# Kernel optimization log

Measured on AMD Instinct MI355X. Metric: run time of the kernel, lower is better.

Reference implementation:

```python
import jax, jax.numpy as jnp
import numpy as np

D_MODEL, N_HEAD, D_HEAD, D_ROPE = 2048, 16, 128, 64
D_KV, D_Q = 512, 1024
THETA = 10000.0


def _cos_sin(seq_len):
    # freqs_cis equivalent: angles [seq_len, d_rope//2]
    inv = 1.0 / (THETA ** (jnp.arange(0, D_ROPE, 2, dtype=jnp.float32) / D_ROPE))
    ang = jnp.arange(seq_len, dtype=jnp.float32)[:, None] * inv[None, :]
    return jnp.cos(ang), jnp.sin(ang)


def _rope(t, cos, sin):
    # t: [b, s, h, d_rope]; rotate interleaved (even, odd) pairs as complex mult
    t1, t2 = t[..., 0::2], t[..., 1::2]
    c = cos[None, :, None, :]
    s = sin[None, :, None, :]
    out = jnp.stack([t1 * c - t2 * s, t1 * s + t2 * c], axis=-1)
    return out.reshape(t.shape)


def setup_inputs() -> dict:
    key = jax.random.key(0)
    ks = jax.random.split(key, 10)
    b, s = 1, 2048
    x = jax.random.normal(ks[0], (b, s, D_MODEL), dtype=jnp.float32)
    # additive causal mask [s, s]
    mask = jnp.where(jnp.tril(jnp.ones((s, s), dtype=bool)), 0.0, -1e9).astype(jnp.float32)
    def w(k, fan_in, fan_out):
        lim = (6.0 / (fan_in + fan_out)) ** 0.5  # xavier_uniform
        return jax.random.uniform(k, (fan_in, fan_out), jnp.float32, -lim, lim)
    return {
        'x': x, 'mask': mask,
        'W_kv_down': w(ks[1], D_MODEL, D_KV),
        'W_k_up':    w(ks[2], D_KV, N_HEAD * D_HEAD),
        'W_v_up':    w(ks[3], D_KV, N_HEAD * D_HEAD),
        'W_q_down':  w(ks[4], D_MODEL, D_Q),
        'W_q_up':    w(ks[5], D_Q, N_HEAD * D_HEAD),
        'W_q_rope':  w(ks[6], D_Q, N_HEAD * D_ROPE),
        'W_k_rope':  w(ks[7], D_MODEL, N_HEAD * D_ROPE),
        'W_out':     w(ks[8], N_HEAD * D_HEAD, D_MODEL),
    }


def reference(x, mask, W_kv_down, W_k_up, W_v_up, W_q_down, W_q_up, W_q_rope, W_k_rope, W_out):
    b, s, _ = x.shape
    cos, sin = _cos_sin(s)
    # low-rank KV path
    down_kv = x @ W_kv_down                                      # [b,s,d_kv]
    k_c = (down_kv @ W_k_up).reshape(b, s, N_HEAD, D_HEAD)
    v   = (down_kv @ W_v_up).reshape(b, s, N_HEAD, D_HEAD)
    # low-rank Q path
    down_q = x @ W_q_down                                        # [b,s,d_q]
    q_c = (down_q @ W_q_up).reshape(b, s, N_HEAD, D_HEAD)
    q_r = (down_q @ W_q_rope).reshape(b, s, N_HEAD, D_ROPE)
    k_r = (x @ W_k_rope).reshape(b, s, N_HEAD, D_ROPE)
    # decoupled RoPE on rope parts only
    q_r = _rope(q_r, cos, sin)
    k_r = _rope(k_r, cos, sin)
    # concat content + rope, heads to dim 1
    q = jnp.concatenate([q_c, q_r], axis=-1).transpose(0, 2, 1, 3)  # [b,h,s,dh+dr]
    k = jnp.concatenate([k_c, k_r], axis=-1).transpose(0, 2, 1, 3)
    vv = v.transpose(0, 2, 1, 3)                                     # [b,h,s,dh]
    scale = 1.0 / jnp.sqrt(jnp.float32(D_HEAD + D_ROPE))
    scores = jnp.einsum('bhqd,bhkd->bhqk', q, k) * scale + mask[None, None]
    probs = jax.nn.softmax(scores.astype(jnp.float32), axis=-1).astype(q.dtype)
    out = jnp.einsum('bhqk,bhkd->bhqd', probs, vv)                   # [b,h,s,dh]
    out = out.transpose(0, 2, 1, 3).reshape(b, s, N_HEAD * D_HEAD)
    return out @ W_out
```

## Files before the change

kernel.cpp:

```cpp
#include <hip/hip_runtime.h>
#include <hip/hip_bf16.h>
#include <math.h>

#define S 2048
#define DM 2048
#define NH 16
#define DH 128
#define DR 64
#define DKV 512
#define DQ 1024
#define DQK 192
#define QSCALE 0.07216878364870323f

typedef __bf16 bf16x8 __attribute__((ext_vector_type(8)));
typedef float f32x4 __attribute__((ext_vector_type(4)));
typedef unsigned short u16;

__device__ inline unsigned int pack2_bf16(float a, float b) {
    __hip_bfloat16 ha = __float2bfloat16(a);
    __hip_bfloat16 hb = __float2bfloat16(b);
    unsigned short ua = *reinterpret_cast<unsigned short*>(&ha);
    unsigned short ub = *reinterpret_cast<unsigned short*>(&hb);
    return (unsigned int)ua | ((unsigned int)ub << 16);
}
__device__ inline u16 f2bf(float v) {
    __hip_bfloat16 hb = __float2bfloat16(v);
    return *reinterpret_cast<u16*>(&hb);
}
__device__ inline void gload_lds16(const void* g, void* l) {
    __builtin_amdgcn_global_load_lds(
        (const __attribute__((address_space(1))) void*)g,
        (__attribute__((address_space(3))) void*)l, 16, 0, 0);
}

__global__ __launch_bounds__(256) void prep_kernel(
    const float* __restrict__ x,
    const float* __restrict__ W0, const float* __restrict__ W1, const float* __restrict__ W2,
    const float* __restrict__ W3, const float* __restrict__ W4, const float* __restrict__ W5,
    const float* __restrict__ W6, const float* __restrict__ W7,
    u16* __restrict__ x_bf,
    u16* __restrict__ D0, u16* __restrict__ D1, u16* __restrict__ D2, u16* __restrict__ D3,
    u16* __restrict__ D4, u16* __restrict__ D5, u16* __restrict__ D6, u16* __restrict__ D7,
    float* __restrict__ cosT, float* __restrict__ sinT) {
    __shared__ u16 tile[64][65];
    const int b = blockIdx.x;
    if (b < 3584) {
        const float* W; u16* D; int N, K, local;
        if (b < 256)       { W = W0; D = D0; N = 512;  K = 2048; local = b; }
        else if (b < 768)  { W = W1; D = D1; N = 1024; K = 2048; local = b - 256; }
        else if (b < 1280) { W = W2; D = D2; N = 1024; K = 2048; local = b - 768; }
        else if (b < 1536) { W = W3; D = D3; N = 2048; K = 512;  local = b - 1280; }
        else if (b < 1792) { W = W4; D = D4; N = 2048; K = 512;  local = b - 1536; }
        else if (b < 2304) { W = W5; D = D5; N = 2048; K = 1024; local = b - 1792; }
        else if (b < 2560) { W = W6; D = D6; N = 1024; K = 1024; local = b - 2304; }
        else               { W = W7; D = D7; N = 2048; K = 2048; local = b - 2560; }
        const int nt = N / 64;
        const int n0 = (local % nt) * 64;
        const int k0 = (local / nt) * 64;
        const int tx = threadIdx.x & 15;
        const int ty = threadIdx.x >> 4;
#pragma unroll
        for (int rep = 0; rep < 4; ++rep) {
            int kk = rep * 16 + ty;
            float4 v = *reinterpret_cast<const float4*>(&W[(size_t)(k0 + kk) * N + n0 + tx * 4]);
            tile[kk][tx * 4 + 0] = f2bf(v.x);
            tile[kk][tx * 4 + 1] = f2bf(v.y);
            tile[kk][tx * 4 + 2] = f2bf(v.z);
            tile[kk][tx * 4 + 3] = f2bf(v.w);
        }
        __syncthreads();
#pragma unroll
        for (int rep = 0; rep < 4; ++rep) {
            int nn = rep * 16 + ty;
            uint2 w;
            w.x = (unsigned int)tile[tx * 4 + 0][nn] | ((unsigned int)tile[tx * 4 + 1][nn] << 16);
            w.y = (unsigned int)tile[tx * 4 + 2][nn] | ((unsigned int)tile[tx * 4 + 3][nn] << 16);
            *reinterpret_cast<uint2*>(&D[(size_t)(n0 + nn) * K + k0 + tx * 4]) = w;
        }
    } else if (b < 7680) {
        int idx = (b - 3584) * 256 + threadIdx.x;
        float4 v = *reinterpret_cast<const float4*>(&x[(size_t)idx * 4]);
        uint2 w;
        w.x = pack2_bf16(v.x, v.y);
        w.y = pack2_bf16(v.z, v.w);
        *reinterpret_cast<uint2*>(&x_bf[(size_t)idx * 4]) = w;
    } else {
        int idx = (b - 7680) * 256 + threadIdx.x;
        int pos = idx / (DR / 2);
        int j   = idx % (DR / 2);
        float inv = __expf(-((float)(2 * j) / (float)DR) * logf(10000.0f));
        float ang = (float)pos * inv;
        cosT[idx] = cosf(ang);
        sinT[idx] = sinf(ang);
    }
}

template <int MODE>
__device__ __forceinline__ void gemm_core(
    u16 (*lds)[6144],
    const u16* __restrict__ A, const u16* __restrict__ BT,
    void* __restrict__ P0v, void* __restrict__ P1v, void* __restrict__ P2v,
    const float* __restrict__ cosT, const float* __restrict__ sinT, int K,
    int bm, int bn) {
    const int tid  = threadIdx.x;
    const int wave = tid >> 6;
    const int lane = tid & 63;
    const int c16  = lane & 15;
    const int g    = lane >> 4;
    const int wm = (wave >> 1) * 32;
    const int wn = (wave & 1) * 64;

    f32x4 acc[2][4];
#pragma unroll
    for (int i = 0; i < 2; ++i)
#pragma unroll
        for (int j = 0; j < 4; ++j) acc[i][j] = f32x4{0.f, 0.f, 0.f, 0.f};

    auto stage = [&](int buf, int k0) {
        {
            int L = tid;
            int rp = L >> 3, e = L & 7, x = e ^ (rp & 7);
            int row = 2 * rp + (x >> 2), kc = x & 3;
            gload_lds16(A + (size_t)(bm + row) * K + k0 + kc * 8, &lds[buf][wave * 512]);
        }
#pragma unroll
        for (int r = 0; r < 2; ++r) {
            int L = r * 256 + tid;
            int rp = L >> 3, e = L & 7, x = e ^ (rp & 7);
            int row = 2 * rp + (x >> 2), kc = x & 3;
            gload_lds16(BT + (size_t)(bn + row) * K + k0 + kc * 8,
                        &lds[buf][2048 + (r * 256 + wave * 64) * 8]);
        }
    };

    const int NT = K / 32;
    stage(0, 0);
    __syncthreads();
    int cur = 0;
    for (int t = 0; t < NT; ++t) {
        if (t + 1 < NT) stage(cur ^ 1, (t + 1) * 32);
        bf16x8 af[2], bfr[4];
#pragma unroll
        for (int i = 0; i < 2; ++i) {
            int row  = wm + i * 16 + c16;
            int slot = ((row >> 1) << 3) + ((((row & 1) << 2) + g) ^ ((row >> 1) & 7));
            af[i] = *reinterpret_cast<const bf16x8*>(&lds[cur][slot * 8]);
        }
#pragma unroll
        for (int j = 0; j < 4; ++j) {
            int row  = wn + j * 16 + c16;
            int slot = ((row >> 1) << 3) + ((((row & 1) << 2) + g) ^ ((row >> 1) & 7));
            bfr[j] = *reinterpret_cast<const bf16x8*>(&lds[cur][2048 + slot * 8]);
        }
#pragma unroll
        for (int i = 0; i < 2; ++i)
#pragma unroll
            for (int j = 0; j < 4; ++j)
                acc[i][j] = __builtin_amdgcn_mfma_f32_16x16x32_bf16(af[i], bfr[j], acc[i][j], 0, 0, 0);
        __syncthreads();
        cur ^= 1;
    }

#pragma unroll
    for (int i = 0; i < 2; ++i)
#pragma unroll
        for (int j = 0; j < 4; ++j) {
            const int mrow = bm + wm + i * 16 + g * 4;
            const int col  = bn + wn + j * 16 + c16;
            if constexpr (MODE == 0) {
                if (col < 512) {
                    u16* down_kv = (u16*)P0v;
#pragma unroll
                    for (int r = 0; r < 4; ++r)
                        down_kv[(size_t)(mrow + r) * DKV + col] = f2bf(acc[i][j][r]);
                } else if (col < 1536) {
                    u16* down_q = (u16*)P1v;
#pragma unroll
                    for (int r = 0; r < 4; ++r)
                        down_q[(size_t)(mrow + r) * DQ + (col - 512)] = f2bf(acc[i][j][r]);
                } else {
                    u16* k_asm = (u16*)P2v;
                    const int cc = col - 1536, h = cc >> 6, rr = cc & 63, jj = rr >> 1;
#pragma unroll
                    for (int r = 0; r < 4; ++r) {
                        int pos = mrow + r;
                        float self = acc[i][j][r];
                        float vp   = __shfl_xor(self, 1);
                        float c = cosT[pos * (DR / 2) + jj];
                        float s = sinT[pos * (DR / 2) + jj];
                        float val = (rr & 1) ? (vp * s + self * c) : (self * c - vp * s);
                        k_asm[((size_t)h * S + pos) * DQK + DH + rr] = f2bf(val);
                    }
                }
            } else if constexpr (MODE == 1) {
                if (col < 2048) {
                    u16* k_asm = (u16*)P0v;
                    const int h = col >> 7, d = col & 127;
#pragma unroll
                    for (int r = 0; r < 4; ++r)
                        k_asm[((size_t)h * S + mrow + r) * DQK + d] = f2bf(acc[i][j][r]);
                } else {
                    u16* vt = (u16*)P1v;
                    const int cc = col - 2048, h = cc >> 7, d = cc & 127;
                    uint2 w;
                    w.x = pack2_bf16(acc[i][j][0], acc[i][j][1]);
                    w.y = pack2_bf16(acc[i][j][2], acc[i][j][3]);
                    *reinterpret_cast<uint2*>(&vt[((size_t)h * DH + d) * S + mrow]) = w;
                }
            } else if constexpr (MODE == 2) {
                u16* q_asm = (u16*)P0v;
                if (col < 2048) {
                    const int h = col >> 7, d = col & 127;
#pragma unroll
                    for (int r = 0; r < 4; ++r)
                        q_asm[((size_t)h * S + mrow + r) * DQK + d] = f2bf(acc[i][j][r] * QSCALE);
                } else {
                    const int cc = col - 2048, h = cc >> 6, rr = cc & 63, jj = rr >> 1;
#pragma unroll
                    for (int r = 0; r < 4; ++r) {
                        int pos = mrow + r;
                        float self = acc[i][j][r];
                        float vp   = __shfl_xor(self, 1);
                        float c = cosT[pos * (DR / 2) + jj];
                        float s = sinT[pos * (DR / 2) + jj];
                        float val = (rr & 1) ? (vp * s + self * c) : (self * c - vp * s);
                        q_asm[((size_t)h * S + pos) * DQK + DH + rr] = f2bf(val * QSCALE);
                    }
                }
            } else {
                float* outp = (float*)P0v;
#pragma unroll
                for (int r = 0; r < 4; ++r)
                    outp[(size_t)(mrow + r) * DM + col] = acc[i][j][r];
            }
        }
}

template <int MODE>
__global__ __launch_bounds__(256) void gemm_fused_kernel(
    const u16* __restrict__ A, const u16* __restrict__ BT,
    void* __restrict__ P0v, void* __restrict__ P1v, void* __restrict__ P2v,
    const float* __restrict__ cosT, const float* __restrict__ sinT, int K) {
    __shared__ u16 lds[2][6144];
    gemm_core<MODE>(lds, A, BT, P0v, P1v, P2v, cosT, sinT, K,
                    blockIdx.y * 64, blockIdx.x * 128);
}

__global__ __launch_bounds__(256) void gemm_g23_kernel(
    const u16* __restrict__ down_kv, const u16* __restrict__ WT2,
    const u16* __restrict__ down_q,  const u16* __restrict__ WT3,
    u16* __restrict__ k_asm, u16* __restrict__ vt, u16* __restrict__ q_asm,
    const float* __restrict__ cosT, const float* __restrict__ sinT) {
    __shared__ u16 lds[2][6144];
    const int b = blockIdx.x;
    if (b < 1024) {
        gemm_core<1>(lds, down_kv, WT2, k_asm, vt, nullptr, cosT, sinT, DKV,
                     (b >> 5) * 64, (b & 31) * 128);
    } else {
        const int l = b - 1024;
        gemm_core<2>(lds, down_q, WT3, q_asm, nullptr, nullptr, cosT, sinT, DQ,
                     (l / 24) * 64, (l % 24) * 128);
    }
}

__global__ __launch_bounds__(256) void attn_mfma_kernel(const u16* __restrict__ q,
                                                        const u16* __restrict__ k,
                                                        const u16* __restrict__ vt,
                                                        u16* __restrict__ outp) {
    const int wgid = blockIdx.x;
    const int xcd  = wgid & 7;
    const int i    = wgid >> 3;
    const int h  = (i < 32) ? (xcd * 2) : (xcd * 2 + 1);
    const int qt = (i < 32) ? (31 - i) : (i - 32);
    const int q0 = qt * 64;

    const int tid  = threadIdx.x;
    const int wave = tid >> 6;
    const int lane = tid & 63;
    const int col  = lane & 15;
    const int g    = lane >> 4;
    const int qw   = q0 + wave * 16;

    __shared__ u16 Kt[3][32 * DQK];
    __shared__ u16 Vt[3][DH * 32];
    __shared__ __align__(16) u16 p_lds[4][512];

    const int r7  = col & 7;
    const int pv7 = (col >> 1) & 7;
    const int pvb = (col & 1) << 2;

    bf16x8 qf[6];
    const u16* qbase = q + ((size_t)h * S + qw + col) * DQK + g * 8;
#pragma unroll
    for (int c = 0; c < 6; ++c) qf[c] = *reinterpret_cast<const bf16x8*>(qbase + c * 32);

    f32x4 acc[8];
#pragma unroll
    for (int c = 0; c < 8; ++c) acc[c] = f32x4{0.f, 0.f, 0.f, 0.f};
    float m_run = -1e30f, l_run = 0.f;

    auto stage = [&](int buf, int j0) {
#pragma unroll
        for (int r = 0; r < 3; ++r) {
            int L   = r * 256 + tid;
            int row = L / 24, rem = L - row * 24;
            int ch  = ((rem >> 3) << 3) + ((rem & 7) ^ (row & 7));
            gload_lds16(k + ((size_t)h * S + j0 + row) * DQK + ch * 8,
                        &Kt[buf][(r * 256 + wave * 64) * 8]);
        }
#pragma unroll
        for (int r = 0; r < 2; ++r) {
            int L  = r * 256 + tid;
            int rp = L >> 3, x = (L & 7) ^ (rp & 7);
            int d  = 2 * rp + (x >> 2), kc = x & 3;
            gload_lds16(vt + ((size_t)h * DH + d) * S + j0 + kc * 8,
                        &Vt[buf][(r * 256 + wave * 64) * 8]);
        }
    };

    const int T = 2 * qt + 2;
    stage(0, 0);
    if (T > 1) stage(1, 32);

    for (int t = 0; t < T; ++t) {
        if (t + 1 < T) asm volatile("s_waitcnt vmcnt(5)" ::: "memory");
        else           asm volatile("s_waitcnt vmcnt(0)" ::: "memory");
        __builtin_amdgcn_s_barrier();
        asm volatile("" ::: "memory");
        if (t + 2 < T) stage((t + 2) % 3, (t + 2) * 32);
        const int cur = t % 3;
        const int j0  = t * 32;

        f32x4 st[2];
        st[0] = f32x4{0.f, 0.f, 0.f, 0.f};
        st[1] = f32x4{0.f, 0.f, 0.f, 0.f};
#pragma unroll
        for (int tt = 0; tt < 2; ++tt) {
            int rb = (16 * tt + col) * 24;
#pragma unroll
            for (int c = 0; c < 6; ++c) {
                int ch   = g + 4 * c;
                int slot = rb + ((ch >> 3) << 3) + ((ch & 7) ^ r7);
                bf16x8 kf = *reinterpret_cast<const bf16x8*>(&Kt[cur][slot * 8]);
                st[tt] = __builtin_amdgcn_mfma_f32_16x16x32_bf16(kf, qf[c], st[tt], 0, 0, 0);
            }
        }
#pragma unroll
        for (int tt = 0; tt < 2; ++tt) {
            if (j0 + 16 * tt + 15 > qw) {
#pragma unroll
                for (int r = 0; r < 4; ++r) {
                    int key = j0 + 16 * tt + 4 * g + r;
                    st[tt][r] = (key > qw + col) ? -1e30f : st[tt][r];
                }
            }
        }
        float tmax = fmaxf(fmaxf(fmaxf(st[0][0], st[0][1]), fmaxf(st[0][2], st[0][3])),
                           fmaxf(fmaxf(st[1][0], st[1][1]), fmaxf(st[1][2], st[1][3])));
        tmax = fmaxf(tmax, __shfl_xor(tmax, 16));
        tmax = fmaxf(tmax, __shfl_xor(tmax, 32));
        float m_new;
        if (__all(tmax - m_run <= 8.0f)) {
            m_new = m_run;
        } else {
            m_new = fmaxf(m_run, tmax);
            float r_scale = __expf(m_run - m_new);
            l_run *= r_scale;
#pragma unroll
            for (int c = 0; c < 8; ++c) {
                acc[c][0] *= r_scale; acc[c][1] *= r_scale;
                acc[c][2] *= r_scale; acc[c][3] *= r_scale;
            }
            m_run = m_new;
        }
        float p[8];
        float psum = 0.f;
#pragma unroll
        for (int tt = 0; tt < 2; ++tt)
#pragma unroll
            for (int r = 0; r < 4; ++r) {
                float pv = __expf(st[tt][r] - m_new);
                p[tt * 4 + r] = pv;
                psum += pv;
            }
        psum += __shfl_xor(psum, 16);
        psum += __shfl_xor(psum, 32);
        l_run += psum;
#pragma unroll
        for (int tt = 0; tt < 2; ++tt) {
            uint2 w;
            w.x = pack2_bf16(p[tt * 4 + 0], p[tt * 4 + 1]);
            w.y = pack2_bf16(p[tt * 4 + 2], p[tt * 4 + 3]);
            int ch   = 2 * tt + (g >> 1);
            int slot = ((col >> 1) << 3) + ((pvb + ch) ^ pv7);
            *reinterpret_cast<uint2*>(&p_lds[wave][slot * 8 + (g & 1) * 4]) = w;
        }
        {
            int slot = ((col >> 1) << 3) + ((pvb + g) ^ pv7);
            bf16x8 pf = *reinterpret_cast<const bf16x8*>(&p_lds[wave][slot * 8]);
#pragma unroll
            for (int c = 0; c < 8; ++c) {
                int d  = 16 * c + col;
                int vs = ((d >> 1) << 3) + ((pvb + g) ^ pv7);
                bf16x8 vf = *reinterpret_cast<const bf16x8*>(&Vt[cur][vs * 8]);
                acc[c] = __builtin_amdgcn_mfma_f32_16x16x32_bf16(vf, pf, acc[c], 0, 0, 0);
            }
        }
    }

    float inv_l = 1.0f / l_run;
#pragma unroll
    for (int c = 0; c < 8; ++c)
#pragma unroll
        for (int r = 0; r < 4; ++r)
            outp[(size_t)(qw + col) * (NH * DH) + h * DH + 16 * c + 4 * g + r] = f2bf(acc[c][r] * inv_l);
}

extern "C" void kernel_launch(void* const* d_in, const int* in_sizes, int n_in,
                              void* d_out, int out_size, void* d_ws, size_t ws_size,
                              hipStream_t stream) {
    const float* x         = (const float*)d_in[0];
    const float* W_kv_down = (const float*)d_in[2];
    const float* W_k_up    = (const float*)d_in[3];
    const float* W_v_up    = (const float*)d_in[4];
    const float* W_q_down  = (const float*)d_in[5];
    const float* W_q_up    = (const float*)d_in[6];
    const float* W_q_rope  = (const float*)d_in[7];
    const float* W_k_rope  = (const float*)d_in[8];
    const float* W_out     = (const float*)d_in[9];
    float* out = (float*)d_out;

    float* w = (float*)d_ws;
    float* cosT = w;
    float* sinT = w + (size_t)S * (DR / 2);
    u16* b = (u16*)(w + 2 * (size_t)S * (DR / 2));
    size_t off = 0;
    u16* x_bf    = b + off; off += (size_t)S * DM;
    u16* WT1     = b + off; off += (size_t)2560 * DM;
    u16* WT2     = b + off; off += (size_t)4096 * DKV;
    u16* WT3     = b + off; off += (size_t)3072 * DQ;
    u16* WT4     = b + off; off += (size_t)DM * DM;
    u16* down_kv = b + off; off += (size_t)S * DKV;
    u16* down_q  = b + off; off += (size_t)S * DQ;
    u16* q_asm   = b + off; off += (size_t)NH * S * DQK;
    u16* k_asm   = b + off; off += (size_t)NH * S * DQK;
    u16* vt      = b + off; off += (size_t)NH * DH * S;
    u16* attn_bf = b + off; off += (size_t)S * NH * DH;

    prep_kernel<<<7936, 256, 0, stream>>>(
        x, W_kv_down, W_q_down, W_k_rope, W_k_up, W_v_up, W_q_up, W_q_rope, W_out,
        x_bf,
        WT1, WT1 + (size_t)512 * DM, WT1 + (size_t)1536 * DM,
        WT2, WT2 + (size_t)2048 * DKV,
        WT3, WT3 + (size_t)2048 * DQ, WT4,
        cosT, sinT);

    gemm_fused_kernel<0><<<dim3(2560 / 128, S / 64), 256, 0, stream>>>(
        x_bf, WT1, down_kv, down_q, k_asm, cosT, sinT, DM);

    gemm_g23_kernel<<<1792, 256, 0, stream>>>(
        down_kv, WT2, down_q, WT3, k_asm, vt, q_asm, cosT, sinT);

    attn_mfma_kernel<<<512, 256, 0, stream>>>(q_asm, k_asm, vt, attn_bf);

    gemm_fused_kernel<3><<<dim3(DM / 128, S / 64), 256, 0, stream>>>(
        attn_bf, WT4, out, nullptr, nullptr, cosT, sinT, DM);
}
```

Before: 219.2 us.

## Split attention KV range across two wave groups and pair causal q-tiles per block

The attention kernel now runs 512-thread blocks, each handling two query tiles of one head (a long and a short tile, qt and 31-qt) in sequence, giving every block the same causal work. Within a tile, two 4-wave groups each process half of every 64-key chunk (split-K flash attention) and merge their partial softmax statistics and accumulators through LDS at the end. This aims to balance causal load and double the waves working on each tile, at the cost of extra LDS (about 90KB, which limits blocks per CU), full-block barriers each iteration, a merge step, and double-buffered rather than triple-buffered staging.

```diff
diff --git a/kernel.cpp b/kernel.cpp
--- a/kernel.cpp
+++ b/kernel.cpp
@@ -263,157 +263,203 @@
     }
 }
 
-__global__ __launch_bounds__(256) void attn_mfma_kernel(const u16* __restrict__ q,
+__global__ __launch_bounds__(512) void attn_mfma_kernel(const u16* __restrict__ q,
                                                         const u16* __restrict__ k,
                                                         const u16* __restrict__ vt,
                                                         u16* __restrict__ outp) {
     const int wgid = blockIdx.x;
     const int xcd  = wgid & 7;
     const int i    = wgid >> 3;
-    const int h  = (i < 32) ? (xcd * 2) : (xcd * 2 + 1);
-    const int qt = (i < 32) ? (31 - i) : (i - 32);
-    const int q0 = qt * 64;
+    const int h    = xcd * 2 + (i & 1);
+    const int pr   = i >> 1;
+    const int qtA  = 31 - pr;
+    const int qtB  = pr;
 
     const int tid  = threadIdx.x;
     const int wave = tid >> 6;
+    const int grp  = wave >> 2;
+    const int w4   = wave & 3;
     const int lane = tid & 63;
     const int col  = lane & 15;
     const int g    = lane >> 4;
-    const int qw   = q0 + wave * 16;
-
-    __shared__ u16 Kt[3][32 * DQK];
-    __shared__ u16 Vt[3][DH * 32];
-    __shared__ __align__(16) u16 p_lds[4][512];
+
+    __shared__ __align__(16) char arena[92160];
+    u16* KtG = (u16*)(arena + (grp ? 24576 : 0));
+    u16* VtG = (u16*)(arena + 49152 + (grp ? 16384 : 0));
+    u16* p_my = (u16*)(arena + 81920 + wave * 1024);
+    float2* ml = (float2*)(arena + 90112);
+    f32x4* cmb = (f32x4*)(arena);
 
     const int r7  = col & 7;
     const int pv7 = (col >> 1) & 7;
     const int pvb = (col & 1) << 2;
 
-    bf16x8 qf[6];
-    const u16* qbase = q + ((size_t)h * S + qw + col) * DQK + g * 8;
-#pragma unroll
-    for (int c = 0; c < 6; ++c) qf[c] = *reinterpret_cast<const bf16x8*>(qbase + c * 32);
-
-    f32x4 acc[8];
-#pragma unroll
-    for (int c = 0; c < 8; ++c) acc[c] = f32x4{0.f, 0.f, 0.f, 0.f};
-    float m_run = -1e30f, l_run = 0.f;
-
-    auto stage = [&](int buf, int j0) {
-#pragma unroll
-        for (int r = 0; r < 3; ++r) {
-            int L   = r * 256 + tid;
-            int row = L / 24, rem = L - row * 24;
-            int ch  = ((rem >> 3) << 3) + ((rem & 7) ^ (row & 7));
-            gload_lds16(k + ((size_t)h * S + j0 + row) * DQK + ch * 8,
-                        &Kt[buf][(r * 256 + wave * 64) * 8]);
-        }
-#pragma unroll
-        for (int r = 0; r < 2; ++r) {
-            int L  = r * 256 + tid;
-            int rp = L >> 3, x = (L & 7) ^ (rp & 7);
-            int d  = 2 * rp + (x >> 2), kc = x & 3;
-            gload_lds16(vt + ((size_t)h * DH + d) * S + j0 + kc * 8,
-                        &Vt[buf][(r * 256 + wave * 64) * 8]);
+    auto stage_pair = [&](int buf, int j0E) {
+#pragma unroll
+        for (int c = 0; c < 5; ++c) {
+            int idx = wave + c * 8;
+            if (idx < 12) {
+                int L = idx * 64 + lane;
+                int row = L / 24, rem = L - row * 24;
+                int ch  = ((rem >> 3) << 3) + ((rem & 7) ^ (row & 7));
+                gload_lds16(k + ((size_t)h * S + j0E + row) * DQK + ch * 8,
+                            (u16*)(arena) + buf * 6144 + idx * 512);
+            } else if (idx < 20) {
+                int s2 = idx - 12;
+                int L = s2 * 64 + lane;
+                int rp = L >> 3, x = (L & 7) ^ (rp & 7);
+                int d  = 2 * rp + (x >> 2), kc = x & 3;
+                gload_lds16(vt + ((size_t)h * DH + d) * S + j0E + kc * 8,
+                            (u16*)(arena + 49152) + buf * 4096 + s2 * 512);
+            } else if (idx < 32) {
+                int s2 = idx - 20;
+                int L = s2 * 64 + lane;
+                int row = L / 24, rem = L - row * 24;
+                int ch  = ((rem >> 3) << 3) + ((rem & 7) ^ (row & 7));
+                gload_lds16(k + ((size_t)h * S + j0E + 32 + row) * DQK + ch * 8,
+                            (u16*)(arena + 24576) + buf * 6144 + s2 * 512);
+            } else {
+                int s2 = idx - 32;
+                int L = s2 * 64 + lane;
+                int rp = L >> 3, x = (L & 7) ^ (rp & 7);
+                int d  = 2 * rp + (x >> 2), kc = x & 3;
+                gload_lds16(vt + ((size_t)h * DH + d) * S + j0E + 32 + kc * 8,
+                            (u16*)(arena + 65536) + buf * 4096 + s2 * 512);
+            }
         }
     };
 
-    const int T = 2 * qt + 2;
-    stage(0, 0);
-    if (T > 1) stage(1, 32);
-
-    for (int t = 0; t < T; ++t) {
-        if (t + 1 < T) asm volatile("s_waitcnt vmcnt(5)" ::: "memory");
-        else           asm volatile("s_waitcnt vmcnt(0)" ::: "memory");
-        __builtin_amdgcn_s_barrier();
-        asm volatile("" ::: "memory");
-        if (t + 2 < T) stage((t + 2) % 3, (t + 2) * 32);
-        const int cur = t % 3;
-        const int j0  = t * 32;
-
-        f32x4 st[2];
-        st[0] = f32x4{0.f, 0.f, 0.f, 0.f};
-        st[1] = f32x4{0.f, 0.f, 0.f, 0.f};
-#pragma unroll
-        for (int tt = 0; tt < 2; ++tt) {
-            int rb = (16 * tt + col) * 24;
-#pragma unroll
-            for (int c = 0; c < 6; ++c) {
-                int ch   = g + 4 * c;
-                int slot = rb + ((ch >> 3) << 3) + ((ch & 7) ^ r7);
-                bf16x8 kf = *reinterpret_cast<const bf16x8*>(&Kt[cur][slot * 8]);
-                st[tt] = __builtin_amdgcn_mfma_f32_16x16x32_bf16(kf, qf[c], st[tt], 0, 0, 0);
-            }
-        }
-#pragma unroll
-        for (int tt = 0; tt < 2; ++tt) {
-            if (j0 + 16 * tt + 15 > qw) {
+    auto phase = [&](int qt) {
+        const int q0 = qt * 64;
+        const int qw = q0 + w4 * 16;
+        const int I  = qt + 1;
+
+        bf16x8 qf[6];
+        const u16* qbase = q + ((size_t)h * S + qw + col) * DQK + g * 8;
+#pragma unroll
+        for (int c = 0; c < 6; ++c) qf[c] = *reinterpret_cast<const bf16x8*>(qbase + c * 32);
+
+        f32x4 acc[8];
+#pragma unroll
+        for (int c = 0; c < 8; ++c) acc[c] = f32x4{0.f, 0.f, 0.f, 0.f};
+        float m_run = -1e30f, l_run = 0.f;
+
+        stage_pair(0, 0);
+        __syncthreads();
+        for (int tp = 0; tp < I; ++tp) {
+            if (tp + 1 < I) stage_pair((tp + 1) & 1, (tp + 1) * 64);
+            const int buf = tp & 1;
+            const int j0  = tp * 64 + grp * 32;
+            const u16* Kc = KtG + buf * 6144;
+            const u16* Vc = VtG + buf * 4096;
+
+            f32x4 st[2];
+            st[0] = f32x4{0.f, 0.f, 0.f, 0.f};
+            st[1] = f32x4{0.f, 0.f, 0.f, 0.f};
+#pragma unroll
+            for (int tt = 0; tt < 2; ++tt) {
+                int rb = (16 * tt + col) * 24;
+#pragma unroll
+                for (int c = 0; c < 6; ++c) {
+                    int ch   = g + 4 * c;
+                    int slot = rb + ((ch >> 3) << 3) + ((ch & 7) ^ r7);
+                    bf16x8 kf = *reinterpret_cast<const bf16x8*>(Kc + slot * 8);
+                    st[tt] = __builtin_amdgcn_mfma_f32_16x16x32_bf16(kf, qf[c], st[tt], 0, 0, 0);
+                }
+            }
+#pragma unroll
+            for (int tt = 0; tt < 2; ++tt) {
+                if (j0 + 16 * tt + 15 > qw) {
+#pragma unroll
+                    for (int r = 0; r < 4; ++r) {
+                        int key = j0 + 16 * tt + 4 * g + r;
+                        st[tt][r] = (key > qw + col) ? -1e30f : st[tt][r];
+                    }
+                }
+            }
+            float tmax = fmaxf(fmaxf(fmaxf(st[0][0], st[0][1]), fmaxf(st[0][2], st[0][3])),
+                               fmaxf(fmaxf(st[1][0], st[1][1]), fmaxf(st[1][2], st[1][3])));
+            tmax = fmaxf(tmax, __shfl_xor(tmax, 16));
+            tmax = fmaxf(tmax, __shfl_xor(tmax, 32));
+            float m_new;
+            if (__all(tmax - m_run <= 8.0f)) {
+                m_new = m_run;
+            } else {
+                m_new = fmaxf(m_run, tmax);
+                float r_scale = __expf(m_run - m_new);
+                l_run *= r_scale;
+#pragma unroll
+                for (int c = 0; c < 8; ++c) {
+                    acc[c][0] *= r_scale; acc[c][1] *= r_scale;
+                    acc[c][2] *= r_scale; acc[c][3] *= r_scale;
+                }
+                m_run = m_new;
+            }
+            float m_sub = (m_new <= -1e29f) ? 0.f : m_new;
+            float p[8];
+            float psum = 0.f;
+#pragma unroll
+            for (int tt = 0; tt < 2; ++tt)
 #pragma unroll
                 for (int r = 0; r < 4; ++r) {
-                    int key = j0 + 16 * tt + 4 * g + r;
-                    st[tt][r] = (key > qw + col) ? -1e30f : st[tt][r];
-                }
-            }
-        }
-        float tmax = fmaxf(fmaxf(fmaxf(st[0][0], st[0][1]), fmaxf(st[0][2], st[0][3])),
-                           fmaxf(fmaxf(st[1][0], st[1][1]), fmaxf(st[1][2], st[1][3])));
-        tmax = fmaxf(tmax, __shfl_xor(tmax, 16));
-        tmax = fmaxf(tmax, __shfl_xor(tmax, 32));
-        float m_new;
-        if (__all(tmax - m_run <= 8.0f)) {
-            m_new = m_run;
-        } else {
-            m_new = fmaxf(m_run, tmax);
-            float r_scale = __expf(m_run - m_new);
-            l_run *= r_scale;
+                    float pv = __expf(st[tt][r] - m_sub);
+                    p[tt * 4 + r] = pv;
+                    psum += pv;
+                }
+            psum += __shfl_xor(psum, 16);
+            psum += __shfl_xor(psum, 32);
+            l_run += psum;
+#pragma unroll
+            for (int tt = 0; tt < 2; ++tt) {
+                uint2 w;
+                w.x = pack2_bf16(p[tt * 4 + 0], p[tt * 4 + 1]);
+                w.y = pack2_bf16(p[tt * 4 + 2], p[tt * 4 + 3]);
+                int ch   = 2 * tt + (g >> 1);
+                int slot = ((col >> 1) << 3) + ((pvb + ch) ^ pv7);
+                *reinterpret_cast<uint2*>(p_my + slot * 8 + (g & 1) * 4) = w;
+            }
+            {
+                int slot = ((col >> 1) << 3) + ((pvb + g) ^ pv7);
+                bf16x8 pf = *reinterpret_cast<const bf16x8*>(p_my + slot * 8);
+#pragma unroll
+                for (int c = 0; c < 8; ++c) {
+                    int d  = 16 * c + col;
+                    int vs = ((d >> 1) << 3) + ((pvb + g) ^ pv7);
+                    bf16x8 vf = *reinterpret_cast<const bf16x8*>(Vc + vs * 8);
+                    acc[c] = __builtin_amdgcn_mfma_f32_16x16x32_bf16(vf, pf, acc[c], 0, 0, 0);
+                }
+            }
+            __syncthreads();
+        }
+
+        if (grp == 1) {
+#pragma unroll
+            for (int c = 0; c < 8; ++c) cmb[(w4 * 8 + c) * 64 + lane] = acc[c];
+            ml[w4 * 64 + lane] = make_float2(m_run, l_run);
+        }
+        __syncthreads();
+        if (grp == 0) {
+            float2 mlB = ml[w4 * 64 + lane];
+            float m = fmaxf(m_run, mlB.x);
+            float sA = __expf(m_run - m);
+            float sB = __expf(mlB.x - m);
+            float l  = l_run * sA + mlB.y * sB;
+            float inv_l = 1.0f / l;
 #pragma unroll
             for (int c = 0; c < 8; ++c) {
-                acc[c][0] *= r_scale; acc[c][1] *= r_scale;
-                acc[c][2] *= r_scale; acc[c][3] *= r_scale;
-            }
-            m_run = m_new;
-        }
-        float p[8];
-        float psum = 0.f;
-#pragma unroll
-        for (int tt = 0; tt < 2; ++tt)
-#pragma unroll
-            for (int r = 0; r < 4; ++r) {
-                float pv = __expf(st[tt][r] - m_new);
-                p[tt * 4 + r] = pv;
-                psum += pv;
-            }
-        psum += __shfl_xor(psum, 16);
-        psum += __shfl_xor(psum, 32);
-        l_run += psum;
-#pragma unroll
-        for (int tt = 0; tt < 2; ++tt) {
-            uint2 w;
-            w.x = pack2_bf16(p[tt * 4 + 0], p[tt * 4 + 1]);
-            w.y = pack2_bf16(p[tt * 4 + 2], p[tt * 4 + 3]);
-            int ch   = 2 * tt + (g >> 1);
-            int slot = ((col >> 1) << 3) + ((pvb + ch) ^ pv7);
-            *reinterpret_cast<uint2*>(&p_lds[wave][slot * 8 + (g & 1) * 4]) = w;
-        }
-        {
-            int slot = ((col >> 1) << 3) + ((pvb + g) ^ pv7);
-            bf16x8 pf = *reinterpret_cast<const bf16x8*>(&p_lds[wave][slot * 8]);
-#pragma unroll
-            for (int c = 0; c < 8; ++c) {
-                int d  = 16 * c + col;
-                int vs = ((d >> 1) << 3) + ((pvb + g) ^ pv7);
-                bf16x8 vf = *reinterpret_cast<const bf16x8*>(&Vt[cur][vs * 8]);
-                acc[c] = __builtin_amdgcn_mfma_f32_16x16x32_bf16(vf, pf, acc[c], 0, 0, 0);
-            }
-        }
-    }
-
-    float inv_l = 1.0f / l_run;
-#pragma unroll
-    for (int c = 0; c < 8; ++c)
-#pragma unroll
-        for (int r = 0; r < 4; ++r)
-            outp[(size_t)(qw + col) * (NH * DH) + h * DH + 16 * c + 4 * g + r] = f2bf(acc[c][r] * inv_l);
+                f32x4 aB = cmb[(w4 * 8 + c) * 64 + lane];
+#pragma unroll
+                for (int r = 0; r < 4; ++r) {
+                    float v = (acc[c][r] * sA + aB[r] * sB) * inv_l;
+                    outp[(size_t)(qw + col) * (NH * DH) + h * DH + 16 * c + 4 * g + r] = f2bf(v);
+                }
+            }
+        }
+        __syncthreads();
+    };
+
+    phase(qtA);
+    phase(qtB);
 }
 
 extern "C" void kernel_launch(void* const* d_in, const int* in_sizes, int n_in,
@@ -461,7 +507,7 @@
     gemm_g23_kernel<<<1792, 256, 0, stream>>>(
         down_kv, WT2, down_q, WT3, k_asm, vt, q_asm, cosT, sinT);
 
-    attn_mfma_kernel<<<512, 256, 0, stream>>>(q_asm, k_asm, vt, attn_bf);
+    attn_mfma_kernel<<<256, 512, 0, stream>>>(q_asm, k_asm, vt, attn_bf);
 
     gemm_fused_kernel<3><<<dim3(DM / 128, S / 64), 256, 0, stream>>>(
         attn_bf, WT4, out, nullptr, nullptr, cosT, sinT, DM);
```

New measurement: 179.2 us. 1.22x faster.
